# Optimization experiments

Measured on AMD Instinct MI355X. Metric: run time of the kernel, lower is better.

## Reference

```python
import jax, jax.numpy as jnp
import numpy as np

NEG = -1.0e9  # large negative number used for causal masking in the original


def setup_inputs() -> dict:
    key = jax.random.key(0)
    ks = jax.random.split(key, 9)
    B, S, D, H = 4, 4096, 512, 64
    sd = 1.0 / np.sqrt(D)
    sh = 1.0 / np.sqrt(H)
    return {
        "x": jax.random.normal(ks[0], (B, S, D), jnp.float32),
        # nn.Linear(d_model, d_head): stored here as (in, out) matrices
        "Wq": jax.random.normal(ks[1], (D, H), jnp.float32) * sd,
        "bq": jax.random.normal(ks[2], (H,), jnp.float32) * 0.01,
        "Wk": jax.random.normal(ks[3], (D, H), jnp.float32) * sd,
        "bk": jax.random.normal(ks[4], (H,), jnp.float32) * 0.01,
        "Wv": jax.random.normal(ks[5], (D, H), jnp.float32) * sd,
        "bv": jax.random.normal(ks[6], (H,), jnp.float32) * 0.01,
        "Wo": jax.random.normal(ks[7], (H, D), jnp.float32) * sh,
        "bo": jax.random.normal(ks[8], (D,), jnp.float32) * 0.01,
    }


def reference(x, Wq, bq, Wk, bk, Wv, bv, Wo, bo):
    # x: (B, S, D)
    B, S, D = x.shape
    Q = x @ Wq + bq  # (B, S, H)
    K = x @ Wk + bk
    V = x @ Wv + bv
    scores = jnp.einsum("bsh,bth->bst", Q, K)  # (B, S, S)
    # NOTE: original divides by sqrt(scores.shape[-1]) == sqrt(seq_len), not sqrt(d_head)
    scores = scores / jnp.sqrt(jnp.asarray(S, scores.dtype))
    # causal mask: strictly-upper-triangular entries get NEG added
    mask = jnp.triu(jnp.full((S, S), NEG, dtype=scores.dtype), k=1)
    attn = jax.nn.softmax(scores + mask[None, :, :], axis=-1)
    out = jnp.einsum("bst,bth->bsh", attn, V)  # (B, S, H)
    return out @ Wo + bo  # (B, S, D)
```

## Files before the change

kernel.cpp:

```cpp
#include <hip/hip_runtime.h>

#define S_LEN 4096
#define NROWS 16384

typedef __attribute__((ext_vector_type(8))) __bf16 bf16x8;
typedef __attribute__((ext_vector_type(8))) unsigned short ushort8;
typedef __attribute__((ext_vector_type(4))) unsigned short ushort4_t;
typedef __attribute__((ext_vector_type(4))) float floatx4;

__device__ __forceinline__ unsigned short f2bf(float f) {
    unsigned int u = __float_as_uint(f);
    unsigned int r = (u + 0x7fffu + ((u >> 16) & 1u)) >> 16;
    return (unsigned short)r;
}

__device__ __forceinline__ float fexp2(float x) {
#if __has_builtin(__builtin_amdgcn_exp2f)
    return __builtin_amdgcn_exp2f(x);
#else
    float r; asm("v_exp_f32 %0, %1" : "=v"(r) : "v"(x)); return r;
#endif
}

__global__ __launch_bounds__(256) void convw_kernel(
    const float* __restrict__ Wq, const float* __restrict__ Wk,
    const float* __restrict__ Wv, const float* __restrict__ Wo,
    unsigned short* __restrict__ WqF, unsigned short* __restrict__ WkF,
    unsigned short* __restrict__ WvF, unsigned short* __restrict__ WoF)
{
    int tid = blockIdx.x * 256 + threadIdx.x;
    {
        const int e = tid & 7, cl = (tid >> 3) & 15, quad = (tid >> 7) & 3;
        const int kc = (tid >> 9) & 15, t = tid >> 13;
        const int n = t * 16 + cl, k = kc * 32 + quad * 8 + e;
        WqF[tid] = f2bf(Wq[k * 64 + n]);
        WkF[tid] = f2bf(Wk[k * 64 + n]);
        WvF[tid] = f2bf(Wv[k * 64 + n]);
    }
    {
        const int e = tid & 7, cl = (tid >> 3) & 15, quad = (tid >> 7) & 3;
        const int h = (tid >> 9) & 1, g = tid >> 10;
        const int n = g * 16 + cl, k = h * 32 + quad * 8 + e;
        WoF[tid] = f2bf(Wo[k * 512 + n]);
    }
}

__global__ __launch_bounds__(192) void qkv_kernel(
    const float* __restrict__ x,
    const unsigned short* __restrict__ WqF, const unsigned short* __restrict__ WkF,
    const unsigned short* __restrict__ WvF,
    const float* __restrict__ bq, const float* __restrict__ bk, const float* __restrict__ bv,
    unsigned short* __restrict__ Qb, unsigned short* __restrict__ KF,
    unsigned short* __restrict__ VF)
{
    __shared__ unsigned short xs[8192];
    const int row0 = blockIdx.x * 16;
    const int tid = threadIdx.x;

    const float* xt = x + (size_t)row0 * 512;
    for (int i = tid; i < 2048; i += 192) {
        float4 v = *(const float4*)(xt + i * 4);
        const int r = i >> 7, k = (i & 127) * 4;
        ushort4_t o;
        o[0] = f2bf(v.x); o[1] = f2bf(v.y); o[2] = f2bf(v.z); o[3] = f2bf(v.w);
        *(ushort4_t*)(xs + (k >> 5) * 512 + ((k >> 3) & 3) * 128 + r * 8 + (k & 7)) = o;
    }
    __syncthreads();

    const int m = tid >> 6;
    const int lane = tid & 63, cl = lane & 15, quad = lane >> 4;
    const unsigned short* WF = (m == 0) ? WqF : (m == 1) ? WkF : WvF;
    const float* bias = (m == 0) ? bq : (m == 1) ? bk : bv;

    floatx4 acc[4];
    #pragma unroll
    for (int t = 0; t < 4; t++) acc[t] = (floatx4){0.f, 0.f, 0.f, 0.f};
    #pragma unroll 2
    for (int kc = 0; kc < 16; kc++) {
        const bf16x8 af = *(const bf16x8*)(const void*)(xs + kc * 512 + lane * 8);
        #pragma unroll
        for (int t = 0; t < 4; t++) {
            const bf16x8 bf = *(const bf16x8*)(const void*)(WF + (size_t)(t * 16 + kc) * 512 + lane * 8);
            acc[t] = __builtin_amdgcn_mfma_f32_16x16x32_bf16(af, bf, acc[t], 0, 0, 0);
        }
    }
    if (m == 0) {
        const float scl = 0.022542110013890054f;
        #pragma unroll
        for (int t = 0; t < 4; t++) {
            const int d = t * 16 + cl;
            const float bd = bias[d];
            #pragma unroll
            for (int r = 0; r < 4; r++)
                Qb[(size_t)(row0 + quad * 4 + r) * 64 + d] = f2bf((acc[t][r] + bd) * scl);
        }
    } else if (m == 1) {
        const int g16 = row0 >> 4;
        #pragma unroll
        for (int t = 0; t < 4; t++) {
            const int d = t * 16 + cl;
            const float bd = bias[d];
            const size_t base = ((size_t)g16 * 8 + (d >> 3)) * 128 + (d & 7);
            #pragma unroll
            for (int r = 0; r < 4; r++)
                KF[base + (quad * 4 + r) * 8] = f2bf(acc[t][r] + bd);
        }
    } else {
        const int b = row0 >> 12, s_base = row0 & 4095;
        #pragma unroll
        for (int t = 0; t < 4; t++) {
            const int d = t * 16 + cl;
            const float bd = bias[d];
            #pragma unroll
            for (int r = 0; r < 4; r++) {
                const int s = s_base + quad * 4 + r;
                const size_t off = (size_t)b * (S_LEN * 64) + (size_t)(s >> 6) * 4096
                                 + ((s >> 5) & 1) * 2048 + t * 512 + cl * 32
                                 + ((s >> 3) & 3) * 8 + (s & 7);
                VF[off] = f2bf(acc[t][r] + bd);
            }
        }
    }
}

#define PSTR 152
__global__ __launch_bounds__(256, 2) void attn_kernel(
    const unsigned short* __restrict__ Qb, const unsigned short* __restrict__ Kb,
    const unsigned short* __restrict__ Vt,
    float* __restrict__ Po, float* __restrict__ Pl)
{
    __shared__ float4 shraw[4][304];
    const int bid = blockIdx.x;
    const int pair = bid >> 2, h = bid & 3;
    const int a = 63 - (pair >> 2);
    const int b = pair & 3;
    const int q0 = a * 64;
    const int nkt = a + 1;
    const int kt0 = (h * nkt) >> 2;
    const int kt1 = ((h + 1) * nkt) >> 2;
    const int tid = threadIdx.x;
    const int w = tid >> 6, lane = tid & 63, cl = lane & 15, quad = lane >> 4;

    const size_t qrow = (size_t)b * S_LEN + q0 + w * 16 + cl;
    const bf16x8 aq0 = *(const bf16x8*)(const void*)(Qb + qrow * 64 + quad * 8);
    const bf16x8 aq1 = *(const bf16x8*)(const void*)(Qb + qrow * 64 + 32 + quad * 8);
    const unsigned short* kbb = Kb + (size_t)b * S_LEN * 64;
    const unsigned short* vbb = Vt + (size_t)b * S_LEN * 64;
    const int qm = q0 + w * 16 + quad * 4;

    float lrow[4];
    floatx4 Oacc[4];
    #pragma unroll
    for (int r = 0; r < 4; r++) lrow[r] = 0.f;
    #pragma unroll
    for (int u = 0; u < 4; u++) Oacc[u] = (floatx4){0.f, 0.f, 0.f, 0.f};

    unsigned short* Pw = (unsigned short*)&shraw[w][0];

    int jt = kt0;
    for (; jt + 1 < kt1; jt += 2) {
        __syncthreads();
        float z[8][4];
        bf16x8 vf[8][2];
        {
            bf16x8 kf[4][2];
            #pragma unroll
            for (int t = 0; t < 4; t++) {
                const unsigned short* kp = kbb + ((size_t)(jt * 4 + t) * 8 + quad) * 128 + cl * 8;
                kf[t][0] = *(const bf16x8*)(const void*)kp;
                kf[t][1] = *(const bf16x8*)(const void*)(kp + 512);
            }
            #pragma unroll
            for (int t = 0; t < 4; t++) {
                floatx4 acc = (floatx4){0.f, 0.f, 0.f, 0.f};
                acc = __builtin_amdgcn_mfma_f32_16x16x32_bf16(aq0, kf[t][0], acc, 0, 0, 0);
                acc = __builtin_amdgcn_mfma_f32_16x16x32_bf16(aq1, kf[t][1], acc, 0, 0, 0);
                #pragma unroll
                for (int r = 0; r < 4; r++) z[t][r] = acc[r];
            }
        }
        #pragma unroll
        for (int u = 0; u < 4; u++) {
            const unsigned short* vp = vbb + (size_t)jt * 4096 + u * 512 + cl * 32 + quad * 8;
            vf[u][0] = *(const bf16x8*)(const void*)vp;
            vf[u][1] = *(const bf16x8*)(const void*)(vp + 2048);
        }
        {
            bf16x8 kf[4][2];
            #pragma unroll
            for (int t = 0; t < 4; t++) {
                const unsigned short* kp = kbb + ((size_t)((jt + 1) * 4 + t) * 8 + quad) * 128 + cl * 8;
                kf[t][0] = *(const bf16x8*)(const void*)kp;
                kf[t][1] = *(const bf16x8*)(const void*)(kp + 512);
            }
            #pragma unroll
            for (int t = 0; t < 4; t++) {
                floatx4 acc = (floatx4){0.f, 0.f, 0.f, 0.f};
                acc = __builtin_amdgcn_mfma_f32_16x16x32_bf16(aq0, kf[t][0], acc, 0, 0, 0);
                acc = __builtin_amdgcn_mfma_f32_16x16x32_bf16(aq1, kf[t][1], acc, 0, 0, 0);
                #pragma unroll
                for (int r = 0; r < 4; r++) z[4 + t][r] = acc[r];
            }
        }
        #pragma unroll
        for (int u = 0; u < 4; u++) {
            const unsigned short* vp = vbb + (size_t)(jt + 1) * 4096 + u * 512 + cl * 32 + quad * 8;
            vf[4 + u][0] = *(const bf16x8*)(const void*)vp;
            vf[4 + u][1] = *(const bf16x8*)(const void*)(vp + 2048);
        }
        if (jt + 1 == nkt - 1) {
            const int j0b = (jt + 1) * 64;
            #pragma unroll
            for (int t = 0; t < 4; t++)
                #pragma unroll
                for (int r = 0; r < 4; r++)
                    if (j0b + t * 16 + cl > qm + r) z[4 + t][r] = -1e30f;
        }
        #pragma unroll
        for (int t = 0; t < 8; t++)
            #pragma unroll
            for (int r = 0; r < 4; r++) z[t][r] = fexp2(z[t][r]);
        #pragma unroll
        for (int r = 0; r < 4; r++)
            lrow[r] += ((z[0][r] + z[1][r]) + (z[2][r] + z[3][r]))
                     + ((z[4][r] + z[5][r]) + (z[6][r] + z[7][r]));
        #pragma unroll
        for (int t = 0; t < 8; t++)
            #pragma unroll
            for (int r = 0; r < 4; r++)
                Pw[(quad * 4 + r) * PSTR + t * 16 + cl] = f2bf(z[t][r]);
        bf16x8 ap0 = *(const bf16x8*)(const void*)(Pw + cl * PSTR + quad * 8);
        bf16x8 ap1 = *(const bf16x8*)(const void*)(Pw + cl * PSTR + 32 + quad * 8);
        bf16x8 ap2 = *(const bf16x8*)(const void*)(Pw + cl * PSTR + 64 + quad * 8);
        bf16x8 ap3 = *(const bf16x8*)(const void*)(Pw + cl * PSTR + 96 + quad * 8);
        #pragma unroll
        for (int u = 0; u < 4; u++) {
            Oacc[u] = __builtin_amdgcn_mfma_f32_16x16x32_bf16(ap0, vf[u][0], Oacc[u], 0, 0, 0);
            Oacc[u] = __builtin_amdgcn_mfma_f32_16x16x32_bf16(ap1, vf[u][1], Oacc[u], 0, 0, 0);
            Oacc[u] = __builtin_amdgcn_mfma_f32_16x16x32_bf16(ap2, vf[4 + u][0], Oacc[u], 0, 0, 0);
            Oacc[u] = __builtin_amdgcn_mfma_f32_16x16x32_bf16(ap3, vf[4 + u][1], Oacc[u], 0, 0, 0);
        }
    }
    if (jt < kt1) {
        bf16x8 kf[4][2], vf[4][2];
        #pragma unroll
        for (int t = 0; t < 4; t++) {
            const unsigned short* kp = kbb + ((size_t)(jt * 4 + t) * 8 + quad) * 128 + cl * 8;
            kf[t][0] = *(const bf16x8*)(const void*)kp;
            kf[t][1] = *(const bf16x8*)(const void*)(kp + 512);
        }
        #pragma unroll
        for (int u = 0; u < 4; u++) {
            const unsigned short* vp = vbb + (size_t)jt * 4096 + u * 512 + cl * 32 + quad * 8;
            vf[u][0] = *(const bf16x8*)(const void*)vp;
            vf[u][1] = *(const bf16x8*)(const void*)(vp + 2048);
        }
        float z[4][4];
        #pragma unroll
        for (int t = 0; t < 4; t++) {
            floatx4 acc = (floatx4){0.f, 0.f, 0.f, 0.f};
            acc = __builtin_amdgcn_mfma_f32_16x16x32_bf16(aq0, kf[t][0], acc, 0, 0, 0);
            acc = __builtin_amdgcn_mfma_f32_16x16x32_bf16(aq1, kf[t][1], acc, 0, 0, 0);
            #pragma unroll
            for (int r = 0; r < 4; r++) z[t][r] = acc[r];
        }
        if (jt == nkt - 1) {
            const int j0 = jt * 64;
            #pragma unroll
            for (int t = 0; t < 4; t++)
                #pragma unroll
                for (int r = 0; r < 4; r++)
                    if (j0 + t * 16 + cl > qm + r) z[t][r] = -1e30f;
        }
        #pragma unroll
        for (int t = 0; t < 4; t++)
            #pragma unroll
            for (int r = 0; r < 4; r++) z[t][r] = fexp2(z[t][r]);
        #pragma unroll
        for (int r = 0; r < 4; r++)
            lrow[r] += ((z[0][r] + z[1][r]) + (z[2][r] + z[3][r]));
        #pragma unroll
        for (int t = 0; t < 4; t++)
            #pragma unroll
            for (int r = 0; r < 4; r++)
                Pw[(quad * 4 + r) * PSTR + t * 16 + cl] = f2bf(z[t][r]);
        bf16x8 ap0 = *(const bf16x8*)(const void*)(Pw + cl * PSTR + quad * 8);
        bf16x8 ap1 = *(const bf16x8*)(const void*)(Pw + cl * PSTR + 32 + quad * 8);
        #pragma unroll
        for (int u = 0; u < 4; u++) {
            Oacc[u] = __builtin_amdgcn_mfma_f32_16x16x32_bf16(ap0, vf[u][0], Oacc[u], 0, 0, 0);
            Oacc[u] = __builtin_amdgcn_mfma_f32_16x16x32_bf16(ap1, vf[u][1], Oacc[u], 0, 0, 0);
        }
    }
    #pragma unroll
    for (int r = 0; r < 4; r++) {
        float s = lrow[r];
        s += __shfl_xor(s, 1, 64);
        s += __shfl_xor(s, 2, 64);
        s += __shfl_xor(s, 4, 64);
        s += __shfl_xor(s, 8, 64);
        lrow[r] = s;
    }
    {
        float* pob = Po + (size_t)bid * 64 * 64;
        #pragma unroll
        for (int u = 0; u < 4; u++)
            #pragma unroll
            for (int r = 0; r < 4; r++)
                pob[(size_t)(w * 16 + quad * 4 + r) * 64 + u * 16 + cl] = Oacc[u][r];
        if (cl == 0) {
            #pragma unroll
            for (int r = 0; r < 4; r++)
                Pl[(size_t)bid * 64 + w * 16 + quad * 4 + r] = lrow[r];
        }
    }
}

__global__ __launch_bounds__(256) void amerge_kernel(
    const float* __restrict__ Po, const float* __restrict__ Pl,
    unsigned short* __restrict__ ObF)
{
    const int pair = blockIdx.x;
    const int a = 63 - (pair >> 2), b = pair & 3;
    const int tid = threadIdx.x;
    const int d0 = (tid & 15) * 4, r0 = tid >> 4;
    const size_t base = (size_t)pair * 4;
    const int h2 = d0 >> 5, qd = (d0 >> 3) & 3, e0 = d0 & 7;
    #pragma unroll
    for (int rr = 0; rr < 4; rr++) {
        const int row = r0 + rr * 16;
        const float L = Pl[(base + 0) * 64 + row] + Pl[(base + 1) * 64 + row]
                      + Pl[(base + 2) * 64 + row] + Pl[(base + 3) * 64 + row];
        const float invL = 1.0f / L;
        const float4 a0 = *(const float4*)(Po + ((base + 0) * 64 + row) * 64 + d0);
        const float4 a1 = *(const float4*)(Po + ((base + 1) * 64 + row) * 64 + d0);
        const float4 a2 = *(const float4*)(Po + ((base + 2) * 64 + row) * 64 + d0);
        const float4 a3 = *(const float4*)(Po + ((base + 3) * 64 + row) * 64 + d0);
        ushort4_t ov;
        ov[0] = f2bf((a0.x + a1.x + a2.x + a3.x) * invL);
        ov[1] = f2bf((a0.y + a1.y + a2.y + a3.y) * invL);
        ov[2] = f2bf((a0.z + a1.z + a2.z + a3.z) * invL);
        ov[3] = f2bf((a0.w + a1.w + a2.w + a3.w) * invL);
        const int blk16 = b * 256 + a * 4 + (row >> 4);
        const size_t idx = (size_t)(blk16 * 2 + h2) * 512 + (qd * 16 + (row & 15)) * 8 + e0;
        *(ushort4_t*)(ObF + idx) = ov;
    }
}

__global__ __launch_bounds__(256) void oproj_kernel(
    const unsigned short* __restrict__ ObF, const unsigned short* __restrict__ WoF,
    const float* __restrict__ bo, float* __restrict__ out)
{
    const int blk = blockIdx.x;
    const int row0 = blk * 16;
    const int tid = threadIdx.x;
    const int w = tid >> 6, lane = tid & 63, cl = lane & 15, quad = lane >> 4;
    const bf16x8 a0 = *(const bf16x8*)(const void*)(ObF + (size_t)(blk * 2 + 0) * 512 + lane * 8);
    const bf16x8 a1 = *(const bf16x8*)(const void*)(ObF + (size_t)(blk * 2 + 1) * 512 + lane * 8);
    #pragma unroll 2
    for (int i = 0; i < 8; i++) {
        const int g = w * 8 + i;
        const int n = g * 16 + cl;
        bf16x8 b0 = *(const bf16x8*)(const void*)(WoF + (size_t)(g * 2 + 0) * 512 + lane * 8);
        bf16x8 b1 = *(const bf16x8*)(const void*)(WoF + (size_t)(g * 2 + 1) * 512 + lane * 8);
        floatx4 acc = (floatx4){0.f, 0.f, 0.f, 0.f};
        acc = __builtin_amdgcn_mfma_f32_16x16x32_bf16(a0, b0, acc, 0, 0, 0);
        acc = __builtin_amdgcn_mfma_f32_16x16x32_bf16(a1, b1, acc, 0, 0, 0);
        const float bod = bo[n];
        #pragma unroll
        for (int r = 0; r < 4; r++)
            out[(size_t)(row0 + quad * 4 + r) * 512 + n] = acc[r] + bod;
    }
}

extern "C" void kernel_launch(void* const* d_in, const int* in_sizes, int n_in,
                              void* d_out, int out_size, void* d_ws, size_t ws_size,
                              hipStream_t stream) {
    const float* x  = (const float*)d_in[0];
    const float* Wq = (const float*)d_in[1];
    const float* bq = (const float*)d_in[2];
    const float* Wk = (const float*)d_in[3];
    const float* bk = (const float*)d_in[4];
    const float* Wv = (const float*)d_in[5];
    const float* bv = (const float*)d_in[6];
    const float* Wo = (const float*)d_in[7];
    const float* bo = (const float*)d_in[8];
    float* out = (float*)d_out;

    unsigned short* Qb  = (unsigned short*)d_ws;
    unsigned short* KF  = Qb + (size_t)NROWS * 64;
    unsigned short* VF  = KF + (size_t)NROWS * 64;
    unsigned short* ObF = VF + (size_t)NROWS * 64;
    unsigned short* WqF = ObF + (size_t)NROWS * 64;
    unsigned short* WkF = WqF + 512 * 64;
    unsigned short* WvF = WkF + 512 * 64;
    unsigned short* WoF = WvF + 512 * 64;
    float* Pl = (float*)(WoF + 512 * 64);
    float* Po = out;

    convw_kernel<<<128, 256, 0, stream>>>(Wq, Wk, Wv, Wo, WqF, WkF, WvF, WoF);
    qkv_kernel<<<1024, 192, 0, stream>>>(x, WqF, WkF, WvF, bq, bk, bv, Qb, KF, VF);
    attn_kernel<<<1024, 256, 0, stream>>>(Qb, KF, VF, Po, Pl);
    amerge_kernel<<<256, 256, 0, stream>>>(Po, Pl, ObF);
    oproj_kernel<<<NROWS / 16, 256, 0, stream>>>(ObF, WoF, bo, out);
}
```

Measured before the change: 151.4 us.

## Fuse split-KV merge into output projection with MFMA-fragment partial layout

```diff
diff --git a/kernel.cpp b/kernel.cpp
--- a/kernel.cpp
+++ b/kernel.cpp
@@ -9,9 +9,9 @@
 typedef __attribute__((ext_vector_type(4))) float floatx4;
 
 __device__ __forceinline__ unsigned short f2bf(float f) {
-    unsigned int u = __float_as_uint(f);
-    unsigned int r = (u + 0x7fffu + ((u >> 16) & 1u)) >> 16;
-    return (unsigned short)r;
+    union { __bf16 h; unsigned short u; } c;
+    c.h = (__bf16)f;
+    return c.u;
 }
 
 __device__ __forceinline__ float fexp2(float x) {
@@ -20,6 +20,13 @@
 #else
     float r; asm("v_exp_f32 %0, %1" : "=v"(r) : "v"(x)); return r;
 #endif
+}
+
+__device__ __forceinline__ bf16x8 cvt_bf16x8(float4 a, float4 b) {
+    bf16x8 v;
+    v[0] = (__bf16)a.x; v[1] = (__bf16)a.y; v[2] = (__bf16)a.z; v[3] = (__bf16)a.w;
+    v[4] = (__bf16)b.x; v[5] = (__bf16)b.y; v[6] = (__bf16)b.z; v[7] = (__bf16)b.w;
+    return v;
 }
 
 __global__ __launch_bounds__(256) void convw_kernel(
@@ -302,12 +309,15 @@
         lrow[r] = s;
     }
     {
-        float* pob = Po + (size_t)bid * 64 * 64;
-        #pragma unroll
-        for (int u = 0; u < 4; u++)
-            #pragma unroll
-            for (int r = 0; r < 4; r++)
-                pob[(size_t)(w * 16 + quad * 4 + r) * 64 + u * 16 + cl] = Oacc[u][r];
+        float* pob = Po + (size_t)bid * 4096 + w * 1024;
+        #pragma unroll
+        for (int u = 0; u < 4; u++) {
+            const int base = (u >> 1) * 512
+                           + (((u & 1) * 2 + (cl >> 3)) * 16 + quad * 4) * 8 + (cl & 7);
+            #pragma unroll
+            for (int r = 0; r < 4; r++)
+                pob[base + r * 8] = Oacc[u][r];
+        }
         if (cl == 0) {
             #pragma unroll
             for (int r = 0; r < 4; r++)
@@ -316,47 +326,43 @@
     }
 }
 
-__global__ __launch_bounds__(256) void amerge_kernel(
+__global__ __launch_bounds__(256) void oproj_kernel(
     const float* __restrict__ Po, const float* __restrict__ Pl,
-    unsigned short* __restrict__ ObF)
-{
-    const int pair = blockIdx.x;
-    const int a = 63 - (pair >> 2), b = pair & 3;
-    const int tid = threadIdx.x;
-    const int d0 = (tid & 15) * 4, r0 = tid >> 4;
-    const size_t base = (size_t)pair * 4;
-    const int h2 = d0 >> 5, qd = (d0 >> 3) & 3, e0 = d0 & 7;
-    #pragma unroll
-    for (int rr = 0; rr < 4; rr++) {
-        const int row = r0 + rr * 16;
-        const float L = Pl[(base + 0) * 64 + row] + Pl[(base + 1) * 64 + row]
-                      + Pl[(base + 2) * 64 + row] + Pl[(base + 3) * 64 + row];
-        const float invL = 1.0f / L;
-        const float4 a0 = *(const float4*)(Po + ((base + 0) * 64 + row) * 64 + d0);
-        const float4 a1 = *(const float4*)(Po + ((base + 1) * 64 + row) * 64 + d0);
-        const float4 a2 = *(const float4*)(Po + ((base + 2) * 64 + row) * 64 + d0);
-        const float4 a3 = *(const float4*)(Po + ((base + 3) * 64 + row) * 64 + d0);
-        ushort4_t ov;
-        ov[0] = f2bf((a0.x + a1.x + a2.x + a3.x) * invL);
-        ov[1] = f2bf((a0.y + a1.y + a2.y + a3.y) * invL);
-        ov[2] = f2bf((a0.z + a1.z + a2.z + a3.z) * invL);
-        ov[3] = f2bf((a0.w + a1.w + a2.w + a3.w) * invL);
-        const int blk16 = b * 256 + a * 4 + (row >> 4);
-        const size_t idx = (size_t)(blk16 * 2 + h2) * 512 + (qd * 16 + (row & 15)) * 8 + e0;
-        *(ushort4_t*)(ObF + idx) = ov;
-    }
-}
-
-__global__ __launch_bounds__(256) void oproj_kernel(
-    const unsigned short* __restrict__ ObF, const unsigned short* __restrict__ WoF,
+    const unsigned short* __restrict__ WoF,
     const float* __restrict__ bo, float* __restrict__ out)
 {
     const int blk = blockIdx.x;
     const int row0 = blk * 16;
+    const int b = row0 >> 12, s0 = row0 & 4095;
+    const int a = s0 >> 6, g16 = (s0 >> 4) & 3;
+    const int pair = (63 - a) * 4 + b;
     const int tid = threadIdx.x;
     const int w = tid >> 6, lane = tid & 63, cl = lane & 15, quad = lane >> 4;
-    const bf16x8 a0 = *(const bf16x8*)(const void*)(ObF + (size_t)(blk * 2 + 0) * 512 + lane * 8);
-    const bf16x8 a1 = *(const bf16x8*)(const void*)(ObF + (size_t)(blk * 2 + 1) * 512 + lane * 8);
+
+    float s0v[8], s1v[8];
+    #pragma unroll
+    for (int e = 0; e < 8; e++) { s0v[e] = 0.f; s1v[e] = 0.f; }
+    #pragma unroll
+    for (int h = 0; h < 4; h++) {
+        const float* p = Po + ((size_t)(pair * 4 + h) * 4 + g16) * 1024 + lane * 8;
+        #pragma unroll
+        for (int e = 0; e < 8; e++) s0v[e] += p[e];
+        #pragma unroll
+        for (int e = 0; e < 8; e++) s1v[e] += p[512 + e];
+    }
+    float L = 0.f;
+    #pragma unroll
+    for (int h = 0; h < 4; h++)
+        L += Pl[(size_t)(pair * 4 + h) * 64 + g16 * 16 + cl];
+    const float invL = 1.0f / L;
+
+    bf16x8 a0, a1;
+    #pragma unroll
+    for (int e = 0; e < 8; e++) {
+        a0[e] = (__bf16)(s0v[e] * invL);
+        a1[e] = (__bf16)(s1v[e] * invL);
+    }
+
     #pragma unroll 2
     for (int i = 0; i < 8; i++) {
         const int g = w * 8 + i;
@@ -390,17 +396,15 @@
     unsigned short* Qb  = (unsigned short*)d_ws;
     unsigned short* KF  = Qb + (size_t)NROWS * 64;
     unsigned short* VF  = KF + (size_t)NROWS * 64;
-    unsigned short* ObF = VF + (size_t)NROWS * 64;
-    unsigned short* WqF = ObF + (size_t)NROWS * 64;
+    unsigned short* WqF = VF + (size_t)NROWS * 64;
     unsigned short* WkF = WqF + 512 * 64;
     unsigned short* WvF = WkF + 512 * 64;
     unsigned short* WoF = WvF + 512 * 64;
     float* Pl = (float*)(WoF + 512 * 64);
-    float* Po = out;
+    float* Po = Pl + (size_t)1024 * 64;
 
     convw_kernel<<<128, 256, 0, stream>>>(Wq, Wk, Wv, Wo, WqF, WkF, WvF, WoF);
     qkv_kernel<<<1024, 192, 0, stream>>>(x, WqF, WkF, WvF, bq, bk, bv, Qb, KF, VF);
     attn_kernel<<<1024, 256, 0, stream>>>(Qb, KF, VF, Po, Pl);
-    amerge_kernel<<<256, 256, 0, stream>>>(Po, Pl, ObF);
-    oproj_kernel<<<NROWS / 16, 256, 0, stream>>>(ObF, WoF, bo, out);
-}
+    oproj_kernel<<<NROWS / 16, 256, 0, stream>>>(Po, Pl, WoF, bo, out);
+}
```

Result: faster. 145.6 us (-3.8%).
